# Optimization experiments

Hardware: AMD Instinct MI355X
Metric: run time of the kernel (lower is better)

## Reference

```python
import jax, jax.numpy as jnp
import numpy as np

B, S, H = 2, 2048, 2048
NH, NKV, HD = 32, 8, 64
G = NH // NKV  # query heads per KV head
SCALE = HD ** -0.5
NEG = -1e9


def setup_inputs() -> dict:
    key = jax.random.key(0)
    ks = jax.random.split(key, 6)
    hidden_states = jax.random.normal(ks[0], (B, S, H), dtype=jnp.float32)
    # causal additive mask, broadcastable over batch and heads
    causal = jnp.tril(jnp.ones((S, S), dtype=bool))
    attention_mask = jnp.where(causal, 0.0, NEG).astype(jnp.float32)[None, None]
    sd = 1.0 / np.sqrt(H)
    wq = jax.random.normal(ks[1], (H, NH * HD), dtype=jnp.float32) * sd
    wk = jax.random.normal(ks[2], (H, NKV * HD), dtype=jnp.float32) * sd
    wv = jax.random.normal(ks[3], (H, NKV * HD), dtype=jnp.float32) * sd
    wo = jax.random.normal(ks[4], (NH * HD, H), dtype=jnp.float32) * sd
    return {"hidden_states": hidden_states, "attention_mask": attention_mask,
            "wq": wq, "wk": wk, "wv": wv, "wo": wo}


def reference(hidden_states, attention_mask, wq, wk, wv, wo):
    b, s, _ = hidden_states.shape
    # projections; group q heads as [b, kv_head, group, s, d] to avoid
    # materializing expanded K/V (same math as expand+matmul)
    q = (hidden_states @ wq).reshape(b, s, NKV, G, HD)
    k = (hidden_states @ wk).reshape(b, s, NKV, HD)
    v = (hidden_states @ wv).reshape(b, s, NKV, HD)
    q = jnp.einsum('bskgd->bkgsd', q)
    k = jnp.einsum('bskd->bksd', k)
    v = jnp.einsum('bskd->bksd', v)
    scores = jnp.einsum('bkgsd,bktd->bkgst', q, k) * SCALE  # [b,kv,G,s,s]
    mask = attention_mask  # [1,1,S,S] broadcastable
    scores = scores + mask[:, :, None] if mask.ndim == 4 else scores + mask
    attn = jax.nn.softmax(scores.astype(jnp.float32), axis=-1).astype(q.dtype)
    out = jnp.einsum('bkgst,bktd->bkgsd', attn, v)
    out = jnp.einsum('bkgsd->bskgd', out).reshape(b, s, NH * HD)
    return out @ wo
```

## Files before the change

### kernel.cpp

```cpp
#include <hip/hip_runtime.h>
#include <hip/hip_bf16.h>
#include <type_traits>


#define B_SZ 2
#define S_LEN 2048
#define HID 2048
#define NHEADS 32
#define NKVH 8
#define HEADD 64
#define QKV_N 3072
#define QK_SCALE 0.18033688f

typedef __attribute__((ext_vector_type(8))) short bf16x8;
typedef __attribute__((ext_vector_type(4))) float f32x4;

__device__ __forceinline__ float bf2f(unsigned short u) {
  union { unsigned int i; float f; } v;
  v.i = ((unsigned int)u) << 16;
  return v.f;
}
__device__ __forceinline__ unsigned short f2bf(float f) {
  union { float f; unsigned int i; } v;
  v.f = f;
  unsigned int r = v.i + 0x7fffu + ((v.i >> 16) & 1u);
  return (unsigned short)(r >> 16);
}
#if __has_builtin(__builtin_amdgcn_exp2f)
__device__ __forceinline__ float exp2v(float x) { return __builtin_amdgcn_exp2f(x); }
#else
__device__ __forceinline__ float exp2v(float x) { return exp2f(x); }
#endif
__device__ __forceinline__ void gload_lds16(const unsigned short* g, unsigned short* l) {
  __builtin_amdgcn_global_load_lds(
      (const __attribute__((address_space(1))) unsigned int*)g,
      (__attribute__((address_space(3))) unsigned int*)l, 16, 0, 0);
}
__device__ __forceinline__ int pv_perm(int s) {
  return (((s >> 2) & 7) << 3) | (((s >> 5) & 1) << 2) | (s & 3);
}

__global__ void cvt_bf16_kernel(const float4* __restrict__ in,
                                ushort4* __restrict__ out, int n4) {
  int i = blockIdx.x * blockDim.x + threadIdx.x;
  if (i >= n4) return;
  float4 v = in[i];
  ushort4 o;
  o.x = f2bf(v.x); o.y = f2bf(v.y); o.z = f2bf(v.z); o.w = f2bf(v.w);
  out[i] = o;
}

__global__ void transpose_w_kernel(const float* __restrict__ wq,
                                   const float* __restrict__ wk,
                                   const float* __restrict__ wv,
                                   const float* __restrict__ wo,
                                   unsigned short* __restrict__ wAllT,
                                   unsigned short* __restrict__ woT) {
  __shared__ float tile[32][33];
  int n0 = blockIdx.x * 32;
  int r0 = blockIdx.y * 32;
  const float* src;
  unsigned short* dst;
  int C, cb, orow;
  float scale;
  if (n0 < 2048)      { src = wq; C = 2048; cb = n0;        orow = n0;        dst = wAllT; scale = QK_SCALE; }
  else if (n0 < 2560) { src = wk; C = 512;  cb = n0 - 2048; orow = n0;        dst = wAllT; scale = 1.0f; }
  else if (n0 < 3072) { src = wv; C = 512;  cb = n0 - 2560; orow = n0;        dst = wAllT; scale = 1.0f; }
  else                { src = wo; C = 2048; cb = n0 - 3072; orow = n0 - 3072; dst = woT;   scale = 1.0f; }
  int x = threadIdx.x, y = threadIdx.y;
#pragma unroll
  for (int i = 0; i < 32; i += 8)
    tile[y + i][x] = src[(size_t)(r0 + y + i) * C + cb + x];
  __syncthreads();
#pragma unroll
  for (int i = 0; i < 32; i += 8)
    dst[(size_t)(orow + y + i) * HID + r0 + x] = f2bf(tile[x][y + i] * scale);
}

__global__ void transpose_v_kernel(const unsigned short* __restrict__ QKV,
                                   unsigned short* __restrict__ Vt) {
  __shared__ unsigned short tile[32][33];
  int s0 = blockIdx.x * 32, d0 = blockIdx.y * 32;
  int bk = blockIdx.z;
  int b = bk >> 3, kvh = bk & 7;
  int x = threadIdx.x, y = threadIdx.y;
#pragma unroll
  for (int i = 0; i < 32; i += 8)
    tile[y + i][x] =
        QKV[(size_t)(b * S_LEN + s0 + y + i) * QKV_N + 2560 + kvh * HEADD + d0 + x];
  __syncthreads();
  int colg = s0 + x;
  int colp = (colg & ~63) | pv_perm(colg & 63);
#pragma unroll
  for (int i = 0; i < 32; i += 8)
    Vt[((size_t)(b * NKVH + kvh) * HEADD + d0 + y + i) * S_LEN + colp] =
        tile[x][y + i];
}

template <typename OutT>
__global__ __launch_bounds__(512, 2) void gemm_qkv_kernel(
    const unsigned short* __restrict__ A, const unsigned short* __restrict__ Bt,
    OutT* __restrict__ C, int N, int K) {
  extern __shared__ unsigned short sm[];
  const int tid = threadIdx.x;
  const int wave = tid >> 6;
  const int lane = tid & 63;
  const int wm = wave >> 2, wn = wave & 3;
  const int rl = lane & 15, g = lane >> 4;
  const int nwg = gridDim.x;
  const int orig = blockIdx.x;
  const int swz = (orig & 7) * (nwg >> 3) + (orig >> 3);
  const int ntn = N / 192;
  const int m0 = (swz / ntn) << 8;
  const int n0 = (swz % ntn) * 192;
  f32x4 acc[8][3] = {};

  size_t aoff[2];
  int aldst[2];
#pragma unroll
  for (int i = 0; i < 2; ++i) {
    int cc = tid + i * 512;
    int row = cc >> 2, slot = cc & 3;
    aoff[i] = (size_t)(m0 + row) * K + ((slot ^ ((row >> 1) & 3)) * 8);
    aldst[i] = cc * 8;
  }
  size_t boff[3];
  int bldst[3];
#pragma unroll
  for (int i = 0; i < 3; ++i) {
    int cc = tid + i * 512;
    int row = cc >> 3, slot = cc & 7;
    boff[i] = (size_t)(n0 + row) * K + ((slot ^ ((row >> 1) & 3)) * 8);
    bldst[i] = cc * 8;
  }
  const int NT = K >> 6;

#pragma unroll
  for (int i = 0; i < 2; ++i) gload_lds16(A + aoff[i], sm + aldst[i]);
#pragma unroll
  for (int i = 0; i < 3; ++i) gload_lds16(Bt + boff[i], sm + 32768 + bldst[i]);
#pragma unroll
  for (int i = 0; i < 2; ++i) gload_lds16(A + aoff[i] + 32, sm + 8192 + aldst[i]);

  int cur = 0;
  for (int t = 0; t < NT; ++t) {
    const int nxt = cur ^ 1;
    const bool st = (t + 1 < NT);
    const size_t k1 = (size_t)(t + 1) << 6;
    unsigned short* An0 = sm + (nxt * 2 + 0) * 8192;
    unsigned short* An1 = sm + (nxt * 2 + 1) * 8192;
    unsigned short* Bn = sm + 32768 + nxt * 12288;
    const unsigned short* Ac0 = sm + (cur * 2 + 0) * 8192;
    const unsigned short* Ac1 = sm + (cur * 2 + 1) * 8192;
    const unsigned short* Bc = sm + 32768 + cur * 12288;
    bf16x8 bA[4], bB[3];
    if (st) {
      gload_lds16(A + aoff[0] + k1, An0 + aldst[0]);
      gload_lds16(A + aoff[1] + k1, An0 + aldst[1]);
    }
    __builtin_amdgcn_sched_barrier(0);
    if (st) asm volatile("s_waitcnt vmcnt(4)" ::: "memory");
    else    asm volatile("s_waitcnt vmcnt(2)" ::: "memory");
    __builtin_amdgcn_s_barrier();
    __builtin_amdgcn_sched_barrier(0);
#pragma unroll
    for (int nb = 0; nb < 3; ++nb) {
      int rw = wn * 48 + nb * 16 + rl;
      bB[nb] = *(const bf16x8*)&Bc[rw * 64 + ((g ^ ((rw >> 1) & 3)) * 8)];
    }
#pragma unroll
    for (int mi = 0; mi < 4; ++mi) {
      int rw = wm * 128 + mi * 16 + rl;
      bA[mi] = *(const bf16x8*)&Ac0[rw * 32 + ((g ^ ((rw >> 1) & 3)) * 8)];
    }
    __builtin_amdgcn_s_setprio(1);
#pragma unroll
    for (int mi = 0; mi < 4; ++mi)
#pragma unroll
      for (int nb = 0; nb < 3; ++nb)
        acc[mi][nb] = __builtin_amdgcn_mfma_f32_16x16x32_bf16(bA[mi], bB[nb],
                                                              acc[mi][nb], 0, 0, 0);
    __builtin_amdgcn_s_setprio(0);
    if (st) {
      gload_lds16(Bt + boff[0] + k1, Bn + bldst[0]);
      gload_lds16(Bt + boff[1] + k1, Bn + bldst[1]);
      gload_lds16(Bt + boff[2] + k1, Bn + bldst[2]);
    }
#pragma unroll
    for (int mi = 0; mi < 4; ++mi) {
      int rw = wm * 128 + 64 + mi * 16 + rl;
      bA[mi] = *(const bf16x8*)&Ac0[rw * 32 + ((g ^ ((rw >> 1) & 3)) * 8)];
    }
    __builtin_amdgcn_s_setprio(1);
#pragma unroll
    for (int mi = 0; mi < 4; ++mi)
#pragma unroll
      for (int nb = 0; nb < 3; ++nb)
        acc[4 + mi][nb] = __builtin_amdgcn_mfma_f32_16x16x32_bf16(bA[mi], bB[nb],
                                                                  acc[4 + mi][nb], 0, 0, 0);
    __builtin_amdgcn_s_setprio(0);
    if (st) {
      gload_lds16(A + aoff[0] + k1 + 32, An1 + aldst[0]);
      gload_lds16(A + aoff[1] + k1 + 32, An1 + aldst[1]);
    }
    __builtin_amdgcn_sched_barrier(0);
    if (st) asm volatile("s_waitcnt vmcnt(7)" ::: "memory");
    else    asm volatile("s_waitcnt vmcnt(0)" ::: "memory");
    __builtin_amdgcn_s_barrier();
    __builtin_amdgcn_sched_barrier(0);
#pragma unroll
    for (int nb = 0; nb < 3; ++nb) {
      int rw = wn * 48 + nb * 16 + rl;
      bB[nb] = *(const bf16x8*)&Bc[rw * 64 + (((4 + g) ^ ((rw >> 1) & 3)) * 8)];
    }
#pragma unroll
    for (int mi = 0; mi < 4; ++mi) {
      int rw = wm * 128 + mi * 16 + rl;
      bA[mi] = *(const bf16x8*)&Ac1[rw * 32 + ((g ^ ((rw >> 1) & 3)) * 8)];
    }
    __builtin_amdgcn_s_setprio(1);
#pragma unroll
    for (int mi = 0; mi < 4; ++mi)
#pragma unroll
      for (int nb = 0; nb < 3; ++nb)
        acc[mi][nb] = __builtin_amdgcn_mfma_f32_16x16x32_bf16(bA[mi], bB[nb],
                                                              acc[mi][nb], 0, 0, 0);
    __builtin_amdgcn_s_setprio(0);
#pragma unroll
    for (int mi = 0; mi < 4; ++mi) {
      int rw = wm * 128 + 64 + mi * 16 + rl;
      bA[mi] = *(const bf16x8*)&Ac1[rw * 32 + ((g ^ ((rw >> 1) & 3)) * 8)];
    }
    __builtin_amdgcn_s_setprio(1);
#pragma unroll
    for (int mi = 0; mi < 4; ++mi)
#pragma unroll
      for (int nb = 0; nb < 3; ++nb)
        acc[4 + mi][nb] = __builtin_amdgcn_mfma_f32_16x16x32_bf16(bA[mi], bB[nb],
                                                                  acc[4 + mi][nb], 0, 0, 0);
    __builtin_amdgcn_s_setprio(0);
    cur = nxt;
  }
#pragma unroll
  for (int mg = 0; mg < 8; ++mg)
#pragma unroll
    for (int nb = 0; nb < 3; ++nb)
#pragma unroll
      for (int r = 0; r < 4; ++r) {
        int row = m0 + wm * 128 + (mg >> 2) * 64 + (mg & 3) * 16 + g * 4 + r;
        int col = n0 + wn * 48 + nb * 16 + rl;
        float v = acc[mg][nb][r];
        if constexpr (std::is_same_v<OutT, unsigned short>)
          C[(size_t)row * N + col] = f2bf(v);
        else
          C[(size_t)row * N + col] = v;
      }
}

template <typename OutT>
__global__ __launch_bounds__(256) void gemm_bt_kernel(
    const unsigned short* __restrict__ A, const unsigned short* __restrict__ Bt,
    OutT* __restrict__ C, int M, int N, int K) {
  __shared__ unsigned short ldsA[3][128 * 32];
  __shared__ unsigned short ldsB[3][128 * 32];
  const int tid = threadIdx.x;
  const int wave = tid >> 6;
  const int lane = tid & 63;
  const int nwg = gridDim.x;
  const int orig = blockIdx.x;
  const int swz = (orig & 7) * (nwg >> 3) + (orig >> 3);
  const int ntn = N >> 7;
  const int m0 = (swz / ntn) << 7;
  const int n0 = (swz % ntn) << 7;
  const int wr = wave >> 1, wc = wave & 1;
  f32x4 acc[4][4] = {};

  size_t offA[2], offB[2];
#pragma unroll
  for (int i = 0; i < 2; ++i) {
    int cc = tid + i * 256;
    int row = cc >> 2, slot = cc & 3;
    int xk = (slot ^ ((row >> 1) & 3)) * 8;
    offA[i] = (size_t)(m0 + row) * K + xk;
    offB[i] = (size_t)(n0 + row) * K + xk;
  }
  const int rl = lane & 15, g = lane >> 4;
  const int nk = K >> 5;
  const int ldsbase = (wave * 64) * 8;

#pragma unroll
  for (int s = 0; s < 2; ++s) {
#pragma unroll
    for (int i = 0; i < 2; ++i) {
      gload_lds16(A + offA[i] + (s << 5), &ldsA[s][ldsbase + i * 256 * 8]);
      gload_lds16(Bt + offB[i] + (s << 5), &ldsB[s][ldsbase + i * 256 * 8]);
    }
  }
  int cur = 0;

  for (int t = 0; t < nk; ++t) {
    __builtin_amdgcn_sched_barrier(0);
    if (t < nk - 1)
      asm volatile("s_waitcnt vmcnt(4)" ::: "memory");
    else
      asm volatile("s_waitcnt vmcnt(0)" ::: "memory");
    __builtin_amdgcn_s_barrier();
    __builtin_amdgcn_sched_barrier(0);
    if (t + 2 < nk) {
      const int k0 = (t + 2) << 5;
      const int nb = (cur + 2 >= 3) ? cur - 1 : cur + 2;
#pragma unroll
      for (int i = 0; i < 2; ++i) {
        gload_lds16(A + offA[i] + k0, &ldsA[nb][ldsbase + i * 256 * 8]);
        gload_lds16(Bt + offB[i] + k0, &ldsB[nb][ldsbase + i * 256 * 8]);
      }
    }
    const int xs = (g ^ ((rl >> 1) & 3)) * 8;
    bf16x8 a[4], b[4];
#pragma unroll
    for (int mi = 0; mi < 4; ++mi)
      a[mi] = *(const bf16x8*)&ldsA[cur][(wr * 64 + mi * 16 + rl) * 32 + xs];
#pragma unroll
    for (int ni = 0; ni < 4; ++ni)
      b[ni] = *(const bf16x8*)&ldsB[cur][(wc * 64 + ni * 16 + rl) * 32 + xs];
#pragma unroll
    for (int mi = 0; mi < 4; ++mi)
#pragma unroll
      for (int ni = 0; ni < 4; ++ni)
        acc[mi][ni] =
            __builtin_amdgcn_mfma_f32_16x16x32_bf16(a[mi], b[ni], acc[mi][ni], 0, 0, 0);
    cur = (cur + 1 == 3) ? 0 : cur + 1;
  }
#pragma unroll
  for (int mi = 0; mi < 4; ++mi)
#pragma unroll
    for (int ni = 0; ni < 4; ++ni)
#pragma unroll
      for (int r = 0; r < 4; ++r) {
        int row = m0 + wr * 64 + mi * 16 + (lane >> 4) * 4 + r;
        int col = n0 + wc * 64 + ni * 16 + (lane & 15);
        float v = acc[mi][ni][r];
        if constexpr (std::is_same_v<OutT, unsigned short>)
          C[(size_t)row * N + col] = f2bf(v);
        else
          C[(size_t)row * N + col] = v;
      }
}

__global__ __launch_bounds__(256) void mfma_attn_kernel(
    const unsigned short* __restrict__ QKV,
    const unsigned short* __restrict__ Vt,
    unsigned short* __restrict__ O) {
  __shared__ unsigned short Ks[2][64 * 64];
  __shared__ unsigned short Vs[2][64 * 64];
  const int head = blockIdx.y, b = blockIdx.z;
  const int kvh = head >> 2;
  const int tid = threadIdx.x;
  const int w = tid >> 6, lane = tid & 63;
  const int c = lane & 15, g = lane >> 4;
  const int srow = tid >> 3, sslot = tid & 7;
  const int xslot = sslot ^ (srow & 7);

  bf16x8 ones_f;
#pragma unroll
  for (int i = 0; i < 8; ++i) ones_f[i] = (short)0x3F80;

  const unsigned short* Ksrc[2];
  const unsigned short* Vsrc[2];
#pragma unroll
  for (int i = 0; i < 2; ++i) {
    int row = srow + i * 32;
    Ksrc[i] = QKV + (size_t)(b * S_LEN + row) * QKV_N + 2048 + kvh * HEADD + xslot * 8;
    Vsrc[i] = Vt + ((size_t)(b * NKVH + kvh) * HEADD + row) * S_LEN + xslot * 8;
  }

#pragma unroll
  for (int i = 0; i < 2; ++i) {
    gload_lds16(Ksrc[i], &Ks[0][(w * 64 + i * 256) * 8]);
    gload_lds16(Vsrc[i], &Vs[0][(w * 64 + i * 256) * 8]);
  }
  __syncthreads();
  int cur = 0;

  for (int ph = 0; ph < 2; ++ph) {
    const int qt = (ph == 0) ? (int)blockIdx.x : (S_LEN / 64 - 1) - (int)blockIdx.x;
    bf16x8 qf[2];
    {
      const unsigned short* qp =
          QKV + (size_t)(b * S_LEN + qt * 64 + w * 16 + c) * QKV_N + head * HEADD +
          g * 8;
      qf[0] = *(const bf16x8*)(qp);
      qf[1] = *(const bf16x8*)(qp + 32);
    }
    f32x4 o_acc[4] = {};
    f32x4 l_acc = {};

    for (int t = 0; t <= qt; ++t) {
      const int kv0 = t * 64;
      const bool has_next = !(ph == 1 && t == qt);
      if (has_next) {
        const int kvn = (t < qt) ? kv0 + 64 : 0;
        const int nb = cur ^ 1;
#pragma unroll
        for (int i = 0; i < 2; ++i) {
          gload_lds16(Ksrc[i] + (size_t)kvn * QKV_N, &Ks[nb][(w * 64 + i * 256) * 8]);
          gload_lds16(Vsrc[i] + kvn, &Vs[nb][(w * 64 + i * 256) * 8]);
        }
      }
      f32x4 s_acc[4] = {};
      __builtin_amdgcn_s_setprio(1);
#pragma unroll
      for (int ks = 0; ks < 2; ++ks)
#pragma unroll
        for (int kn = 0; kn < 4; ++kn) {
          bf16x8 kf = *(const bf16x8*)&Ks[cur][(kn * 16 + c) * 64 +
                                              (((ks * 4 + g) ^ (c & 7)) * 8)];
          s_acc[kn] =
              __builtin_amdgcn_mfma_f32_16x16x32_bf16(kf, qf[ks], s_acc[kn], 0, 0, 0);
        }
      __builtin_amdgcn_s_setprio(0);
      if (t == qt) {
        const int qg = qt * 64 + w * 16 + c;
#pragma unroll
        for (int kn = 0; kn < 4; ++kn)
#pragma unroll
          for (int r = 0; r < 4; ++r)
            if (kv0 + kn * 16 + g * 4 + r > qg) s_acc[kn][r] = -1e30f;
      }
      float p[4][4];
#pragma unroll
      for (int kn = 0; kn < 4; ++kn)
#pragma unroll
        for (int r = 0; r < 4; ++r)
          p[kn][r] = exp2v(s_acc[kn][r]);
      union { bf16x8 v; unsigned int w4[4]; } afu[2];
#pragma unroll
      for (int b2 = 0; b2 < 2; ++b2) {
        afu[b2].w4[0] = __builtin_amdgcn_perm(__float_as_uint(p[b2][1]),
                                              __float_as_uint(p[b2][0]), 0x07060302u);
        afu[b2].w4[1] = __builtin_amdgcn_perm(__float_as_uint(p[b2][3]),
                                              __float_as_uint(p[b2][2]), 0x07060302u);
        afu[b2].w4[2] = __builtin_amdgcn_perm(__float_as_uint(p[2 + b2][1]),
                                              __float_as_uint(p[2 + b2][0]), 0x07060302u);
        afu[b2].w4[3] = __builtin_amdgcn_perm(__float_as_uint(p[2 + b2][3]),
                                              __float_as_uint(p[2 + b2][2]), 0x07060302u);
      }
      __builtin_amdgcn_s_setprio(1);
#pragma unroll
      for (int ks2 = 0; ks2 < 2; ++ks2) {
#pragma unroll
        for (int dn = 0; dn < 4; ++dn) {
          bf16x8 vf = *(const bf16x8*)&Vs[cur][(dn * 16 + c) * 64 +
                                              (((ks2 * 4 + g) ^ (c & 7)) * 8)];
          o_acc[dn] =
              __builtin_amdgcn_mfma_f32_16x16x32_bf16(afu[ks2].v, vf, o_acc[dn], 0, 0, 0);
        }
        l_acc = __builtin_amdgcn_mfma_f32_16x16x32_bf16(afu[ks2].v, ones_f, l_acc, 0, 0, 0);
      }
      __builtin_amdgcn_s_setprio(0);
      __syncthreads();
      if (has_next) cur ^= 1;
    }
#pragma unroll
    for (int r = 0; r < 4; ++r) {
      float inv = 1.0f / l_acc[r];
      int row = qt * 64 + w * 16 + g * 4 + r;
#pragma unroll
      for (int dn = 0; dn < 4; ++dn) {
        int col = head * HEADD + dn * 16 + c;
        O[(size_t)(b * S_LEN + row) * (NHEADS * HEADD) + col] =
            f2bf(o_acc[dn][r] * inv);
      }
    }
  }
}

extern "C" void kernel_launch(void* const* d_in, const int* in_sizes, int n_in,
                              void* d_out, int out_size, void* d_ws, size_t ws_size,
                              hipStream_t stream) {
  const float* hs = (const float*)d_in[0];
  const float* wq = (const float*)d_in[2];
  const float* wk = (const float*)d_in[3];
  const float* wv = (const float*)d_in[4];
  const float* wo = (const float*)d_in[5];
  float* out = (float*)d_out;

  hipFuncSetAttribute(reinterpret_cast<const void*>(gemm_qkv_kernel<unsigned short>),
                      hipFuncAttributeMaxDynamicSharedMemorySize, 114688);

  char* ws = (char*)d_ws;
  unsigned short* hs_bf = (unsigned short*)(ws);
  unsigned short* wAllT = (unsigned short*)(ws + ((size_t)16 << 20));
  unsigned short* woT  = (unsigned short*)(ws + ((size_t)28 << 20));
  unsigned short* QKV  = (unsigned short*)(ws + ((size_t)36 << 20));
  unsigned short* Ab   = (unsigned short*)(ws + ((size_t)60 << 20));
  unsigned short* VtB  = (unsigned short*)(ws + ((size_t)76 << 20));

  int n4 = (B_SZ * S_LEN * HID) / 4;
  cvt_bf16_kernel<<<n4 / 256, 256, 0, stream>>>((const float4*)hs, (ushort4*)hs_bf, n4);

  dim3 tb(32, 8);
  transpose_w_kernel<<<dim3(160, 64), tb, 0, stream>>>(wq, wk, wv, wo, wAllT, woT);

  gemm_qkv_kernel<unsigned short><<<256, 512, 114688, stream>>>(
      hs_bf, wAllT, QKV, QKV_N, HID);

  transpose_v_kernel<<<dim3(S_LEN / 32, HEADD / 32, B_SZ * NKVH), tb, 0, stream>>>(
      QKV, VtB);

  mfma_attn_kernel<<<dim3(S_LEN / 128, NHEADS, B_SZ), 256, 0, stream>>>(QKV, VtB, Ab);

  gemm_bt_kernel<float><<<32 * 16, 256, 0, stream>>>(
      Ab, woT, out, B_SZ * S_LEN, HID, HID);
}
```

Baseline: 182.8 us.

## Restructure output projection GEMM to 256x128 tiles with 8 waves and K=64 steps

Replaces the 128x128, 4-wave, 3-stage output-projection GEMM with a 256x128 tile computed by 512 threads. Each K-step is 64 wide, split into two half-steps, with double-buffered dynamic LDS and the loads for the next step interleaved between the halves. It also raises wave priority around the MFMA blocks. The aim is more reuse of B per tile, fewer barriers per K, and better overlap of loads with compute. The cost is fewer workgroups (256) and larger LDS use, which may reduce occupancy.

```diff
diff --git a/kernel.cpp b/kernel.cpp
--- a/kernel.cpp
+++ b/kernel.cpp
@@ -258,88 +258,129 @@
 }
 
 template <typename OutT>
-__global__ __launch_bounds__(256) void gemm_bt_kernel(
+__global__ __launch_bounds__(512, 2) void gemm_out_kernel(
     const unsigned short* __restrict__ A, const unsigned short* __restrict__ Bt,
-    OutT* __restrict__ C, int M, int N, int K) {
-  __shared__ unsigned short ldsA[3][128 * 32];
-  __shared__ unsigned short ldsB[3][128 * 32];
+    OutT* __restrict__ C, int N, int K) {
+  extern __shared__ unsigned short sm[];
   const int tid = threadIdx.x;
   const int wave = tid >> 6;
   const int lane = tid & 63;
+  const int wm = wave >> 1, wn = wave & 1;
+  const int rl = lane & 15, g = lane >> 4;
   const int nwg = gridDim.x;
   const int orig = blockIdx.x;
   const int swz = (orig & 7) * (nwg >> 3) + (orig >> 3);
   const int ntn = N >> 7;
-  const int m0 = (swz / ntn) << 7;
+  const int m0 = (swz / ntn) << 8;
   const int n0 = (swz % ntn) << 7;
-  const int wr = wave >> 1, wc = wave & 1;
   f32x4 acc[4][4] = {};
 
-  size_t offA[2], offB[2];
+  size_t aoff[2];
+  int aldst[2];
 #pragma unroll
   for (int i = 0; i < 2; ++i) {
-    int cc = tid + i * 256;
+    int cc = tid + i * 512;
     int row = cc >> 2, slot = cc & 3;
-    int xk = (slot ^ ((row >> 1) & 3)) * 8;
-    offA[i] = (size_t)(m0 + row) * K + xk;
-    offB[i] = (size_t)(n0 + row) * K + xk;
-  }
-  const int rl = lane & 15, g = lane >> 4;
-  const int nk = K >> 5;
-  const int ldsbase = (wave * 64) * 8;
-
-#pragma unroll
-  for (int s = 0; s < 2; ++s) {
-#pragma unroll
-    for (int i = 0; i < 2; ++i) {
-      gload_lds16(A + offA[i] + (s << 5), &ldsA[s][ldsbase + i * 256 * 8]);
-      gload_lds16(Bt + offB[i] + (s << 5), &ldsB[s][ldsbase + i * 256 * 8]);
-    }
-  }
+    aoff[i] = (size_t)(m0 + row) * K + ((slot ^ ((row >> 1) & 3)) * 8);
+    aldst[i] = cc * 8;
+  }
+  size_t boff[2];
+  int bldst[2];
+#pragma unroll
+  for (int i = 0; i < 2; ++i) {
+    int cc = tid + i * 512;
+    int row = cc >> 3, slot = cc & 7;
+    boff[i] = (size_t)(n0 + row) * K + ((slot ^ ((row >> 1) & 3)) * 8);
+    bldst[i] = cc * 8;
+  }
+  const int NT = K >> 6;
+
+#pragma unroll
+  for (int i = 0; i < 2; ++i) gload_lds16(A + aoff[i], sm + aldst[i]);
+#pragma unroll
+  for (int i = 0; i < 2; ++i) gload_lds16(Bt + boff[i], sm + 32768 + bldst[i]);
+#pragma unroll
+  for (int i = 0; i < 2; ++i) gload_lds16(A + aoff[i] + 32, sm + 8192 + aldst[i]);
+
   int cur = 0;
-
-  for (int t = 0; t < nk; ++t) {
-    __builtin_amdgcn_sched_barrier(0);
-    if (t < nk - 1)
-      asm volatile("s_waitcnt vmcnt(4)" ::: "memory");
-    else
-      asm volatile("s_waitcnt vmcnt(0)" ::: "memory");
+  for (int t = 0; t < NT; ++t) {
+    const int nxt = cur ^ 1;
+    const bool st = (t + 1 < NT);
+    const size_t k1 = (size_t)(t + 1) << 6;
+    unsigned short* An0 = sm + (nxt * 2 + 0) * 8192;
+    unsigned short* An1 = sm + (nxt * 2 + 1) * 8192;
+    unsigned short* Bn = sm + 32768 + nxt * 8192;
+    const unsigned short* Ac0 = sm + (cur * 2 + 0) * 8192;
+    const unsigned short* Ac1 = sm + (cur * 2 + 1) * 8192;
+    const unsigned short* Bc = sm + 32768 + cur * 8192;
+    bf16x8 bA[4], bB[4];
+    if (st) {
+      gload_lds16(A + aoff[0] + k1, An0 + aldst[0]);
+      gload_lds16(A + aoff[1] + k1, An0 + aldst[1]);
+    }
+    __builtin_amdgcn_sched_barrier(0);
+    if (st) asm volatile("s_waitcnt vmcnt(4)" ::: "memory");
+    else    asm volatile("s_waitcnt vmcnt(2)" ::: "memory");
     __builtin_amdgcn_s_barrier();
     __builtin_amdgcn_sched_barrier(0);
-    if (t + 2 < nk) {
-      const int k0 = (t + 2) << 5;
-      const int nb = (cur + 2 >= 3) ? cur - 1 : cur + 2;
-#pragma unroll
-      for (int i = 0; i < 2; ++i) {
-        gload_lds16(A + offA[i] + k0, &ldsA[nb][ldsbase + i * 256 * 8]);
-        gload_lds16(Bt + offB[i] + k0, &ldsB[nb][ldsbase + i * 256 * 8]);
-      }
-    }
-    const int xs = (g ^ ((rl >> 1) & 3)) * 8;
-    bf16x8 a[4], b[4];
+#pragma unroll
+    for (int nb = 0; nb < 4; ++nb) {
+      int rw = wn * 64 + nb * 16 + rl;
+      bB[nb] = *(const bf16x8*)&Bc[rw * 64 + ((g ^ ((rw >> 1) & 3)) * 8)];
+    }
+#pragma unroll
+    for (int mi = 0; mi < 4; ++mi) {
+      int rw = wm * 64 + mi * 16 + rl;
+      bA[mi] = *(const bf16x8*)&Ac0[rw * 32 + ((g ^ ((rw >> 1) & 3)) * 8)];
+    }
+    __builtin_amdgcn_s_setprio(1);
 #pragma unroll
     for (int mi = 0; mi < 4; ++mi)
-      a[mi] = *(const bf16x8*)&ldsA[cur][(wr * 64 + mi * 16 + rl) * 32 + xs];
-#pragma unroll
-    for (int ni = 0; ni < 4; ++ni)
-      b[ni] = *(const bf16x8*)&ldsB[cur][(wc * 64 + ni * 16 + rl) * 32 + xs];
+#pragma unroll
+      for (int nb = 0; nb < 4; ++nb)
+        acc[mi][nb] = __builtin_amdgcn_mfma_f32_16x16x32_bf16(bA[mi], bB[nb],
+                                                              acc[mi][nb], 0, 0, 0);
+    __builtin_amdgcn_s_setprio(0);
+    if (st) {
+      gload_lds16(Bt + boff[0] + k1, Bn + bldst[0]);
+      gload_lds16(Bt + boff[1] + k1, Bn + bldst[1]);
+      gload_lds16(A + aoff[0] + k1 + 32, An1 + aldst[0]);
+      gload_lds16(A + aoff[1] + k1 + 32, An1 + aldst[1]);
+    }
+    __builtin_amdgcn_sched_barrier(0);
+    if (st) asm volatile("s_waitcnt vmcnt(6)" ::: "memory");
+    else    asm volatile("s_waitcnt vmcnt(0)" ::: "memory");
+    __builtin_amdgcn_s_barrier();
+    __builtin_amdgcn_sched_barrier(0);
+#pragma unroll
+    for (int nb = 0; nb < 4; ++nb) {
+      int rw = wn * 64 + nb * 16 + rl;
+      bB[nb] = *(const bf16x8*)&Bc[rw * 64 + (((4 + g) ^ ((rw >> 1) & 3)) * 8)];
+    }
+#pragma unroll
+    for (int mi = 0; mi < 4; ++mi) {
+      int rw = wm * 64 + mi * 16 + rl;
+      bA[mi] = *(const bf16x8*)&Ac1[rw * 32 + ((g ^ ((rw >> 1) & 3)) * 8)];
+    }
+    __builtin_amdgcn_s_setprio(1);
 #pragma unroll
     for (int mi = 0; mi < 4; ++mi)
 #pragma unroll
-      for (int ni = 0; ni < 4; ++ni)
-        acc[mi][ni] =
-            __builtin_amdgcn_mfma_f32_16x16x32_bf16(a[mi], b[ni], acc[mi][ni], 0, 0, 0);
-    cur = (cur + 1 == 3) ? 0 : cur + 1;
+      for (int nb = 0; nb < 4; ++nb)
+        acc[mi][nb] = __builtin_amdgcn_mfma_f32_16x16x32_bf16(bA[mi], bB[nb],
+                                                              acc[mi][nb], 0, 0, 0);
+    __builtin_amdgcn_s_setprio(0);
+    cur = nxt;
   }
 #pragma unroll
   for (int mi = 0; mi < 4; ++mi)
 #pragma unroll
-    for (int ni = 0; ni < 4; ++ni)
+    for (int nb = 0; nb < 4; ++nb)
 #pragma unroll
       for (int r = 0; r < 4; ++r) {
-        int row = m0 + wr * 64 + mi * 16 + (lane >> 4) * 4 + r;
-        int col = n0 + wc * 64 + ni * 16 + (lane & 15);
-        float v = acc[mi][ni][r];
+        int row = m0 + wm * 64 + mi * 16 + g * 4 + r;
+        int col = n0 + wn * 64 + nb * 16 + rl;
+        float v = acc[mi][nb][r];
         if constexpr (std::is_same_v<OutT, unsigned short>)
           C[(size_t)row * N + col] = f2bf(v);
         else
@@ -487,6 +528,8 @@
 
   hipFuncSetAttribute(reinterpret_cast<const void*>(gemm_qkv_kernel<unsigned short>),
                       hipFuncAttributeMaxDynamicSharedMemorySize, 114688);
+  hipFuncSetAttribute(reinterpret_cast<const void*>(gemm_out_kernel<float>),
+                      hipFuncAttributeMaxDynamicSharedMemorySize, 98304);
 
   char* ws = (char*)d_ws;
   unsigned short* hs_bf = (unsigned short*)(ws);
@@ -510,6 +553,6 @@
 
   mfma_attn_kernel<<<dim3(S_LEN / 128, NHEADS, B_SZ), 256, 0, stream>>>(QKV, VtB, Ab);
 
-  gemm_bt_kernel<float><<<32 * 16, 256, 0, stream>>>(
-      Ab, woT, out, B_SZ * S_LEN, HID, HID);
-}
+  gemm_out_kernel<float><<<256, 512, 98304, stream>>>(
+      Ab, woT, out, HID, HID);
+}
```

Result: faster. 174.2 us (-4.7%).
